# Kernel optimization log

Measured on AMD Instinct MI355X. Metric: run time of the kernel, lower is better.

Reference implementation:

```python
import jax, jax.numpy as jnp
import numpy as np

DEPTH = 4
DIM = 768
HEADS = 12
DH = 64
INNER = HEADS * DH            # 768
FF_INNER = int(4 * (2.0 / 3.0) * DIM)  # 2048 (GEGLU paper sizing)
B, N = 4, 1024                # N must be a perfect square (2D rotary)
ATTN_SCALE = 8.0              # cosine-sim attention scale from Attention(scale=8)
EPS = 1e-5


def _ln(x, gamma, beta):
    mu = jnp.mean(x, axis=-1, keepdims=True)
    var = jnp.mean((x - mu) ** 2, axis=-1, keepdims=True)
    return (x - mu) * jax.lax.rsqrt(var + EPS) * gamma + beta


def _rope_angles(n, dh):
    # precompute_freqs_cis_2d: x/y positions on sqrt(n) grid, dh//4 freqs each, interleaved
    H = int(n ** 0.5)
    pos = jnp.arange(n)
    xp = (pos % H).astype(jnp.float32)
    yp = (pos // H).astype(jnp.float32)
    freqs = 1.0 / (10000.0 ** (jnp.arange(0, dh, 4)[: dh // 4].astype(jnp.float32) / dh))
    xa = jnp.outer(xp, freqs)  # [n, dh//4]
    ya = jnp.outer(yp, freqs)
    return jnp.stack([xa, ya], axis=-1).reshape(n, dh // 2)  # [n, dh//2]


def _apply_rope(t, cos, sin):
    # t: [B, N, H, DH]; complex-pair rotation on last dim
    tr = t.reshape(*t.shape[:-1], DH // 2, 2)
    r, im = tr[..., 0], tr[..., 1]
    c = cos[None, :, None, :]
    s = sin[None, :, None, :]
    out = jnp.stack([r * c - im * s, r * s + im * c], axis=-1)
    return out.reshape(t.shape)


def _l2norm(t):
    return t / jnp.maximum(jnp.linalg.norm(t, axis=-1, keepdims=True), 1e-12)


def setup_inputs() -> dict:
    key = jax.random.key(0)
    ks = jax.random.split(key, 10)
    w = 0.02
    return {
        "x": jax.random.normal(ks[0], (B, N, DIM), dtype=jnp.float32),
        "attn_gamma": jnp.ones((DEPTH, DIM), dtype=jnp.float32),
        "wq": w * jax.random.normal(ks[1], (DEPTH, DIM, INNER), dtype=jnp.float32),
        "wkv": w * jax.random.normal(ks[2], (DEPTH, DIM, 2 * INNER), dtype=jnp.float32),
        "q_scale": jnp.ones((DEPTH, DH), dtype=jnp.float32),
        "k_scale": jnp.ones((DEPTH, DH), dtype=jnp.float32),
        "wo": w * jax.random.normal(ks[3], (DEPTH, INNER, DIM), dtype=jnp.float32),
        "ff_gamma": jnp.ones((DEPTH, DIM), dtype=jnp.float32),
        "ff_beta": jnp.zeros((DEPTH, DIM), dtype=jnp.float32),
        "wff1": w * jax.random.normal(ks[4], (DEPTH, DIM, 2 * FF_INNER), dtype=jnp.float32),
        "wff2": w * jax.random.normal(ks[5], (DEPTH, FF_INNER, DIM), dtype=jnp.float32),
    }


def reference(x, attn_gamma, wq, wkv, q_scale, k_scale, wo, ff_gamma, ff_beta, wff1, wff2):
    b, n, _ = x.shape
    ang = _rope_angles(n, DH)
    cos, sin = jnp.cos(ang), jnp.sin(ang)
    for i in range(DEPTH):
        # ---- Attention (qk-l2norm cosine attention, 2D rotary, scale=8) ----
        h = _ln(x, attn_gamma[i], 0.0)          # Attention.norm (beta is a zero buffer)
        kv_in = x                                # faithful: kv_input taken BEFORE norm
        q = (h @ wq[i]).reshape(b, n, HEADS, DH)
        kv = kv_in @ wkv[i]
        k, v = jnp.split(kv, 2, axis=-1)
        k = k.reshape(b, n, HEADS, DH)
        v = v.reshape(b, n, HEADS, DH)
        q = _apply_rope(q, cos, sin)
        k = _apply_rope(k, cos, sin)
        q = jnp.transpose(q, (0, 2, 1, 3))       # b h n d
        k = jnp.transpose(k, (0, 2, 1, 3))
        v = jnp.transpose(v, (0, 2, 1, 3))
        q = _l2norm(q) * q_scale[i]
        k = _l2norm(k) * k_scale[i]
        sim = jnp.einsum('bhid,bhjd->bhij', q, k) * ATTN_SCALE
        attn = jax.nn.softmax(sim, axis=-1)
        o = jnp.einsum('bhij,bhjd->bhid', attn, v)
        o = jnp.transpose(o, (0, 2, 1, 3)).reshape(b, n, INNER)
        x = x + o @ wo[i]
        # ---- GEGLU FeedForward ----
        hf = _ln(x, ff_gamma[i], ff_beta[i])
        u = hf @ wff1[i]
        a, g = jnp.split(u, 2, axis=-1)
        x = x + (a * jax.nn.gelu(g, approximate=False)) @ wff2[i]
    return x
```

## Files before the change

kernel.cpp:

```cpp
#include <hip/hip_runtime.h>
#include <hip/hip_bf16.h>
#include <math.h>

typedef __hip_bfloat16 bf16;
typedef __bf16 bf16x8 __attribute__((ext_vector_type(8)));
typedef float f32x4 __attribute__((ext_vector_type(4)));

#define NDEPTH 4
#define DIM 768
#define HEADS 12
#define DH 64
#define INNER 768
#define FFI 2048
#define BB 4
#define NN 1024
#define ROWS (BB*NN)

__device__ __forceinline__ void async_cp16(const bf16* g, bf16* l) {
  __builtin_amdgcn_global_load_lds(
      (const __attribute__((address_space(1))) unsigned int*)g,
      (__attribute__((address_space(3))) unsigned int*)l, 16, 0, 0);
}

template<int BN, bool GELU, bool VOUT, int K, int LD>
__device__ __forceinline__ void gemm_body(
    const bf16* __restrict__ A, const bf16* __restrict__ Bt,
    bf16* __restrict__ Cb, float* __restrict__ Cf, const float* __restrict__ Rf,
    bf16* __restrict__ Vt, int M, int N, int bx, int by, bf16* As, bf16* Bs)
{
  constexpr int WN = BN / 2;
  constexpr int NT = WN / 16;
  const int tid  = threadIdx.x;
  const int lane = tid & 63, w = tid >> 6;
  const int quad = lane >> 4, l16 = lane & 15;
  const int wr = w >> 1, wc = w & 1;
  const int m0 = by * 128, n0 = bx * BN;

  f32x4 acc[4][NT] = {};

  constexpr int CHA = 128 * 8;
  constexpr int CH  = CHA + BN * 8;
  constexpr int NCH = CH / 256;
  constexpr int NTK = K / 64;

  auto stage = [&](int kk, int buf) {
    bf16* Asb = As + buf * (128*64);
    bf16* Bsb = Bs + buf * (BN*64);
    #pragma unroll
    for (int t = 0; t < NCH; ++t) {
      int c0 = w*64 + t*256;
      int ch = c0 + lane;
      if (c0 < CHA) {
        int r = ch >> 3, j = (ch & 7) ^ (r & 7);
        async_cp16(&A[(size_t)(m0 + r)*LD + kk + j*8], &Asb[(size_t)c0*8]);
      } else {
        int ch2 = ch - CHA, r = ch2 >> 3, j = (ch2 & 7) ^ (r & 7);
        async_cp16(&Bt[(size_t)(n0 + r)*LD + kk + j*8], &Bsb[(size_t)(c0 - CHA)*8]);
      }
    }
  };

  stage(0, 0);
  __syncthreads();

  #pragma unroll
  for (int t = 0; t < NTK; ++t) {
    const int buf = t & 1;
    if (t + 1 < NTK) stage((t + 1) * 64, buf ^ 1);

    const bf16* Asb = As + buf * (128*64);
    const bf16* Bsb = Bs + buf * (BN*64);

    #pragma unroll
    for (int kc = 0; kc < 2; ++kc) {
      bf16x8 bfr[NT];
      #pragma unroll
      for (int nt = 0; nt < NT; ++nt) {
        int rb = wc*WN + nt*16 + l16;
        int c  = (kc*4 + quad) ^ (rb & 7);
        bfr[nt] = *(const bf16x8*)&Bsb[rb*64 + c*8];
      }
      #pragma unroll
      for (int mt = 0; mt < 4; ++mt) {
        int ra = wr*64 + mt*16 + l16;
        int ca = (kc*4 + quad) ^ (ra & 7);
        bf16x8 af = *(const bf16x8*)&Asb[ra*64 + ca*8];
        #pragma unroll
        for (int nt = 0; nt < NT; ++nt)
          acc[mt][nt] = __builtin_amdgcn_mfma_f32_16x16x32_bf16(af, bfr[nt], acc[mt][nt], 0, 0, 0);
      }
    }
    if (t + 1 < NTK) __syncthreads();
  }

  #pragma unroll
  for (int mt = 0; mt < 4; ++mt) {
    #pragma unroll
    for (int nt = 0; nt < NT; ++nt) {
      int row = m0 + wr*64 + mt*16 + quad*4;
      int col = n0 + wc*WN + nt*16 + l16;
      if (GELU) {
        #pragma unroll
        for (int r = 0; r < 4; ++r) {
          float v = acc[mt][nt][r];
          float g = __shfl_xor(v, 1);
          if (!(lane & 1)) {
            float ge = 0.5f * g * (1.f + erff(g * 0.70710678118654752f));
            Cb[(size_t)(row + r)*(N >> 1) + (col >> 1)] = __float2bfloat16(v * ge);
          }
        }
      } else if (VOUT) {
        if (col < INNER) {
          #pragma unroll
          for (int r = 0; r < 4; ++r)
            Cb[(size_t)(row + r)*INNER + col] = __float2bfloat16(acc[mt][nt][r]);
        } else {
          int c2 = col - INNER, hh = c2 >> 6, d = c2 & 63;
          int b = row >> 10, nn = row & 1023;
          union { ushort4 u4; bf16 h4[4]; } p;
          #pragma unroll
          for (int r = 0; r < 4; ++r) p.h4[r] = __float2bfloat16(acc[mt][nt][r]);
          *(ushort4*)&Vt[(((size_t)b*HEADS + hh)*DH + d)*NN + nn] = p.u4;
        }
      } else {
        #pragma unroll
        for (int r = 0; r < 4; ++r) {
          float v = acc[mt][nt][r];
          size_t idx = (size_t)(row + r) * N + col;
          if (Rf) v += Rf[idx];
          if (Cf) Cf[idx] = v;
          if (Cb) Cb[idx] = __float2bfloat16(v);
        }
      }
    }
  }
}

template<int BN, bool GELU, int K, int LD>
__global__ __launch_bounds__(256) void gemm_kernel(
    const bf16* __restrict__ A, const bf16* __restrict__ Bt,
    bf16* __restrict__ Cb, float* __restrict__ Cf, const float* __restrict__ Rf,
    int M, int N)
{
  __shared__ __align__(16) bf16 As[2*128*64];
  __shared__ __align__(16) bf16 Bs[2*BN*64];
  gemm_body<BN,GELU,false,K,LD>(A, Bt, Cb, Cf, Rf, nullptr, M, N,
                                blockIdx.x, blockIdx.y, As, Bs);
}

template<int BN, int KH, int LD>
__global__ __launch_bounds__(256) void gemm_splitk_kernel(
    const bf16* __restrict__ A, const bf16* __restrict__ Bt,
    float* __restrict__ P, int M, int N)
{
  __shared__ __align__(16) bf16 As[2*128*64];
  __shared__ __align__(16) bf16 Bs[2*BN*64];
  const int z = blockIdx.z;
  gemm_body<BN,false,false,KH,LD>(A + (size_t)z*KH, Bt + (size_t)z*KH, nullptr,
                                  P + (size_t)z*M*N, nullptr, nullptr,
                                  M, N, blockIdx.x, blockIdx.y, As, Bs);
}

__global__ __launch_bounds__(256) void qkv_kernel(
    const bf16* __restrict__ h, const bf16* __restrict__ x16,
    const bf16* __restrict__ wqT, const bf16* __restrict__ wkvT,
    bf16* __restrict__ qb, bf16* __restrict__ kb, bf16* __restrict__ vt)
{
  __shared__ __align__(16) bf16 As[2*128*64];
  __shared__ __align__(16) bf16 Bs[2*128*64];
  if (blockIdx.z == 0)
    gemm_body<64,false,false,768,768>(h, wqT, qb, nullptr, nullptr, nullptr,
                                      ROWS, INNER, blockIdx.x, blockIdx.y, As, Bs);
  else
    gemm_body<128,false,true,768,768>(x16, wkvT, kb, nullptr, nullptr, vt,
                                      ROWS, 2*INNER, blockIdx.x, blockIdx.y, As, Bs);
}

__global__ __launch_bounds__(256) void ln_kernel(
    const float* __restrict__ x, const float* __restrict__ g,
    const float* __restrict__ bta, bf16* __restrict__ out)
{
  const int row = blockIdx.x, tid = threadIdx.x;
  const size_t base = (size_t)row * DIM;
  float v[3];
  #pragma unroll
  for (int j = 0; j < 3; ++j) v[j] = x[base + tid + j*256];
  float s  = v[0] + v[1] + v[2];
  float ss = v[0]*v[0] + v[1]*v[1] + v[2]*v[2];
  #pragma unroll
  for (int off = 32; off; off >>= 1) { s += __shfl_xor(s, off); ss += __shfl_xor(ss, off); }
  __shared__ float red[8];
  int w = tid >> 6;
  if ((tid & 63) == 0) { red[w] = s; red[w + 4] = ss; }
  __syncthreads();
  s  = red[0] + red[1] + red[2] + red[3];
  ss = red[4] + red[5] + red[6] + red[7];
  float mean = s * (1.f/768.f);
  float var  = ss * (1.f/768.f) - mean*mean;
  float rstd = rsqrtf(fmaxf(var, 0.f) + 1e-5f);
  #pragma unroll
  for (int j = 0; j < 3; ++j) {
    int c = tid + j*256;
    float bv = bta ? bta[c] : 0.f;
    out[base + c] = __float2bfloat16((v[j] - mean) * rstd * g[c] + bv);
  }
}

__global__ __launch_bounds__(256) void redln_kernel(
    const float* __restrict__ P0, const float* __restrict__ P1,
    const float* __restrict__ res,
    float* __restrict__ xo32, bf16* __restrict__ xo16, float* __restrict__ outf,
    const float* __restrict__ g, const float* __restrict__ bta,
    bf16* __restrict__ lnout)
{
  const int row = blockIdx.x, tid = threadIdx.x;
  const size_t base = (size_t)row * DIM;
  float v[3];
  #pragma unroll
  for (int j = 0; j < 3; ++j) {
    size_t idx = base + tid + j*256;
    v[j] = res[idx] + P0[idx] + P1[idx];
    if (xo32) xo32[idx] = v[j];
    if (xo16) xo16[idx] = __float2bfloat16(v[j]);
    if (outf) outf[idx] = v[j];
  }
  if (!g) return;
  float s  = v[0] + v[1] + v[2];
  float ss = v[0]*v[0] + v[1]*v[1] + v[2]*v[2];
  #pragma unroll
  for (int off = 32; off; off >>= 1) { s += __shfl_xor(s, off); ss += __shfl_xor(ss, off); }
  __shared__ float red[8];
  int w = tid >> 6;
  if ((tid & 63) == 0) { red[w] = s; red[w + 4] = ss; }
  __syncthreads();
  s  = red[0] + red[1] + red[2] + red[3];
  ss = red[4] + red[5] + red[6] + red[7];
  float mean = s * (1.f/768.f);
  float var  = ss * (1.f/768.f) - mean*mean;
  float rstd = rsqrtf(fmaxf(var, 0.f) + 1e-5f);
  #pragma unroll
  for (int j = 0; j < 3; ++j) {
    int c = tid + j*256;
    float bv = bta ? bta[c] : 0.f;
    lnout[base + c] = __float2bfloat16((v[j] - mean) * rstd * g[c] + bv);
  }
}

__global__ __launch_bounds__(384) void rope_kernel(
    const bf16* __restrict__ q, const bf16* __restrict__ kb,
    const float* __restrict__ qsc, const float* __restrict__ ksc,
    bf16* __restrict__ qh, bf16* __restrict__ kh)
{
  const int bn = blockIdx.x;
  const int b = bn >> 10, n = bn & 1023;
  const int tid = threadIdx.x;
  const int h = tid >> 5, pr = tid & 31, d0 = pr*2;
  const float xp = (float)(n & 31), yp = (float)(n >> 5);
  const int t = pr >> 1;
  const float freq = powf(10000.f, -(float)t / 16.f);
  const float ang = (pr & 1) ? yp * freq : xp * freq;
  float sn, cs;
  sincosf(ang, &sn, &cs);
  const float2 qs2 = *(const float2*)&qsc[d0];
  const float2 ks2 = *(const float2*)&ksc[d0];

  union { unsigned int u; bf16 h2[2]; } qa, ka, qo, ko;
  qa.u = *(const unsigned int*)&q [(size_t)bn*INNER + h*64 + d0];
  ka.u = *(const unsigned int*)&kb[(size_t)bn*INNER + h*64 + d0];
  float qre = __bfloat162float(qa.h2[0]), qim = __bfloat162float(qa.h2[1]);
  float kre = __bfloat162float(ka.h2[0]), kim = __bfloat162float(ka.h2[1]);
  float qr = qre*cs - qim*sn, qi = qre*sn + qim*cs;
  float kr = kre*cs - kim*sn, ki = kre*sn + kim*cs;
  float q2 = qr*qr + qi*qi, k2 = kr*kr + ki*ki;
  #pragma unroll
  for (int off = 1; off < 32; off <<= 1) { q2 += __shfl_xor(q2, off); k2 += __shfl_xor(k2, off); }
  float qinv = 8.f / fmaxf(sqrtf(q2), 1e-12f);
  float kinv = 1.f / fmaxf(sqrtf(k2), 1e-12f);
  qo.h2[0] = __float2bfloat16(qr * qinv * qs2.x);
  qo.h2[1] = __float2bfloat16(qi * qinv * qs2.y);
  ko.h2[0] = __float2bfloat16(kr * kinv * ks2.x);
  ko.h2[1] = __float2bfloat16(ki * kinv * ks2.y);
  size_t oi = (((size_t)b*HEADS + h)*NN + n)*DH + d0;
  *(unsigned int*)&qh[oi] = qo.u;
  *(unsigned int*)&kh[oi] = ko.u;
}

__global__ __launch_bounds__(256) void attn_kernel(
    const bf16* __restrict__ qh, const bf16* __restrict__ kh,
    const bf16* __restrict__ vt, const float* __restrict__ qsc,
    const float* __restrict__ ksc, bf16* __restrict__ ob)
{
  __shared__ __align__(16) bf16 Qs[64*72];
  __shared__ __align__(16) bf16 Ks[64*72];
  __shared__ __align__(16) bf16 Vt[64*72];
  __shared__ __align__(16) bf16 Ps[4][16*72];

  const int tid = threadIdx.x;
  const int lane = tid & 63, w = tid >> 6;
  const int quad = lane >> 4, l16 = lane & 15;
  const int qt = blockIdx.x, bh = blockIdx.y;
  const int b = bh / HEADS, h = bh % HEADS;
  const size_t base = (size_t)bh * NN * DH;

  float mq = fabsf(qsc[lane]), mk = fabsf(ksc[lane]);
  #pragma unroll
  for (int off = 1; off < 64; off <<= 1) {
    mq = fmaxf(mq, __shfl_xor(mq, off));
    mk = fmaxf(mk, __shfl_xor(mk, off));
  }
  const float Mb = 8.f * mq * mk;

  for (int c = tid; c < 512; c += 256) {
    int r = c >> 3, j = c & 7;
    *(uint4*)&Qs[r*72 + j*8] = *(const uint4*)&qh[base + (size_t)(qt*64 + r)*64 + j*8];
  }

  f32x4 o[4] = {};
  float pl[4] = {0.f, 0.f, 0.f, 0.f};

  for (int kt0 = 0; kt0 < NN/64; ++kt0) {
    __syncthreads();
    for (int c = tid; c < 512; c += 256) {
      int r = c >> 3, j = c & 7;
      *(uint4*)&Ks[r*72 + j*8] = *(const uint4*)&kh[base + (size_t)(kt0*64 + r)*64 + j*8];
      *(uint4*)&Vt[r*72 + j*8] = *(const uint4*)&vt[base + (size_t)r*NN + kt0*64 + j*8];
    }
    __syncthreads();

    f32x4 s[4] = {};
    bf16x8 aq[2];
    #pragma unroll
    for (int kc = 0; kc < 2; ++kc)
      aq[kc] = *(const bf16x8*)&Qs[(w*16 + l16)*72 + kc*32 + quad*8];
    #pragma unroll
    for (int kt = 0; kt < 4; ++kt)
      #pragma unroll
      for (int kc = 0; kc < 2; ++kc) {
        bf16x8 bk = *(const bf16x8*)&Ks[(kt*16 + l16)*72 + kc*32 + quad*8];
        s[kt] = __builtin_amdgcn_mfma_f32_16x16x32_bf16(aq[kc], bk, s[kt], 0, 0, 0);
      }

    #pragma unroll
    for (int r = 0; r < 4; ++r) {
      #pragma unroll
      for (int kt = 0; kt < 4; ++kt) {
        float pv = __expf(s[kt][r] - Mb);
        pl[r] += pv;
        Ps[w][(quad*4 + r)*72 + kt*16 + l16] = __float2bfloat16(pv);
      }
    }
    __syncthreads();

    #pragma unroll
    for (int kc = 0; kc < 2; ++kc) {
      bf16x8 ap = *(const bf16x8*)&Ps[w][l16*72 + kc*32 + quad*8];
      #pragma unroll
      for (int nt = 0; nt < 4; ++nt) {
        bf16x8 bv = *(const bf16x8*)&Vt[(nt*16 + l16)*72 + kc*32 + quad*8];
        o[nt] = __builtin_amdgcn_mfma_f32_16x16x32_bf16(ap, bv, o[nt], 0, 0, 0);
      }
    }
  }

  float l[4];
  #pragma unroll
  for (int r = 0; r < 4; ++r) {
    float rs = pl[r];
    #pragma unroll
    for (int off = 1; off < 16; off <<= 1) rs += __shfl_xor(rs, off);
    l[r] = rs;
  }

  #pragma unroll
  for (int nt = 0; nt < 4; ++nt)
    #pragma unroll
    for (int r = 0; r < 4; ++r) {
      int n = qt*64 + w*16 + quad*4 + r;
      int dcol = nt*16 + l16;
      ob[((size_t)(b*NN + n)*HEADS + h)*DH + dcol] = __float2bfloat16(o[nt][r] / l[r]);
    }
}

__global__ __launch_bounds__(256) void cast_kernel(
    const float* __restrict__ x, bf16* __restrict__ o)
{
  size_t i = ((size_t)blockIdx.x*256 + threadIdx.x) * 8;
  float4 f0 = *(const float4*)(x + i);
  float4 f1 = *(const float4*)(x + i + 4);
  union { uint4 u; bf16 h[8]; } p;
  p.h[0] = __float2bfloat16(f0.x); p.h[1] = __float2bfloat16(f0.y);
  p.h[2] = __float2bfloat16(f0.z); p.h[3] = __float2bfloat16(f0.w);
  p.h[4] = __float2bfloat16(f1.x); p.h[5] = __float2bfloat16(f1.y);
  p.h[6] = __float2bfloat16(f1.z); p.h[7] = __float2bfloat16(f1.w);
  *(uint4*)(o + i) = p.u;
}

struct TD { const float* src; bf16* dst; int R, C, base, perm; };
struct TDs5 { TD d[5]; };

__global__ __launch_bounds__(256) void wtrans_kernel(TDs5 a)
{
  const int blk = blockIdx.x;
  int di = 0;
  #pragma unroll
  for (int k = 1; k < 5; ++k) if (blk >= a.d[k].base) di = k;
  const TD d = a.d[di];
  const int local = blk - d.base;
  const int tilesX = d.C >> 5;
  const int by = local / tilesX, bx = local - by*tilesX;
  __shared__ float t[32][33];
  const int tx = threadIdx.x & 31, ty = threadIdx.x >> 5;
  const int c0 = bx*32, r0 = by*32;
  #pragma unroll
  for (int i = 0; i < 4; ++i)
    t[ty + i*8][tx] = d.src[(size_t)(r0 + ty + i*8)*d.C + c0 + tx];
  __syncthreads();
  const int half = d.C >> 1;
  #pragma unroll
  for (int i = 0; i < 4; ++i) {
    int c = c0 + ty + i*8;
    int rout = d.perm ? ((c < half) ? 2*c : 2*(c - half) + 1) : c;
    d.dst[(size_t)rout*d.R + r0 + tx] = __float2bfloat16(t[tx][ty + i*8]);
  }
}

extern "C" void kernel_launch(void* const* d_in, const int* in_sizes, int n_in,
                              void* d_out, int out_size, void* d_ws, size_t ws_size,
                              hipStream_t stream)
{
  const float* x_in       = (const float*)d_in[0];
  const float* attn_gamma = (const float*)d_in[1];
  const float* wq         = (const float*)d_in[2];
  const float* wkv        = (const float*)d_in[3];
  const float* q_scale    = (const float*)d_in[4];
  const float* k_scale    = (const float*)d_in[5];
  const float* wo         = (const float*)d_in[6];
  const float* ff_gamma   = (const float*)d_in[7];
  const float* ff_beta    = (const float*)d_in[8];
  const float* wff1       = (const float*)d_in[9];
  const float* wff2       = (const float*)d_in[10];
  float* outp = (float*)d_out;
  char* ws = (char*)d_ws;

  const size_t E = (size_t)ROWS * DIM;
  float* xw32 = (float*)ws;
  bf16*  xw16 = (bf16*)(ws + 12582912);
  bf16*  S_h  = (bf16*)(ws + 18874368);
  char*  BIGb = ws + 25165824;
  bf16*  WT   = (bf16*)(ws + 62914560);
  bf16*  qbuf  = (bf16*)BIGb;
  bf16*  kbuf  = qbuf + E;
  bf16*  qhb   = qbuf + 2*E;
  bf16*  khb   = qbuf + 3*E;
  bf16*  vtb   = qbuf + 4*E;
  bf16*  glbuf = (bf16*)BIGb;
  float* wP    = (float*)BIGb;
  float* fP    = (float*)(BIGb + 16777216);
  bf16*  wqT   = WT;
  bf16*  wkvT  = WT + 589824;
  bf16*  woT   = WT + 1769472;
  bf16*  wff1T = WT + 2359296;
  bf16*  wff2T = WT + 5505024;

  cast_kernel<<<1536, 256, 0, stream>>>(x_in, xw16);
  ln_kernel<<<ROWS, 256, 0, stream>>>(x_in, attn_gamma, nullptr, S_h);

  for (int i = 0; i < NDEPTH; ++i) {
    const float* xsrc = (i == 0) ? x_in : xw32;

    TDs5 td;
    td.d[0] = { wq   + (size_t)i*589824,  wqT,   768,  768,    0, 0 };
    td.d[1] = { wkv  + (size_t)i*1179648, wkvT,  768, 1536,  576, 0 };
    td.d[2] = { wo   + (size_t)i*589824,  woT,   768,  768, 1728, 0 };
    td.d[3] = { wff1 + (size_t)i*3145728, wff1T, 768, 4096, 2304, 1 };
    td.d[4] = { wff2 + (size_t)i*1572864, wff2T, 2048, 768, 5376, 0 };
    wtrans_kernel<<<6912, 256, 0, stream>>>(td);

    qkv_kernel<<<dim3(12,32,2), 256, 0, stream>>>(S_h, xw16, wqT, wkvT, qbuf, kbuf, vtb);
    rope_kernel<<<ROWS, 384, 0, stream>>>(qbuf, kbuf, q_scale + i*DH, k_scale + i*DH, qhb, khb);
    attn_kernel<<<dim3(16,48), 256, 0, stream>>>(qhb, khb, vtb,
                                                 q_scale + i*DH, k_scale + i*DH, S_h);
    gemm_splitk_kernel<64,384,768><<<dim3(12,32,2), 256, 0, stream>>>(S_h, woT, wP, ROWS, DIM);
    redln_kernel<<<ROWS, 256, 0, stream>>>(wP, wP + E, xsrc, xw32, nullptr, nullptr,
                                           ff_gamma + i*DIM, ff_beta + i*DIM, S_h);
    gemm_kernel<128,true,768,768><<<dim3(32,32), 256, 0, stream>>>(S_h, wff1T, glbuf, nullptr, nullptr, ROWS, 2*FFI);
    gemm_splitk_kernel<64,1024,2048><<<dim3(12,32,2), 256, 0, stream>>>(glbuf, wff2T, fP, ROWS, DIM);
    if (i < NDEPTH-1)
      redln_kernel<<<ROWS, 256, 0, stream>>>(fP, fP + E, xw32, xw32, xw16, nullptr,
                                             attn_gamma + (i+1)*DIM, nullptr, S_h);
    else
      redln_kernel<<<ROWS, 256, 0, stream>>>(fP, fP + E, xw32, nullptr, nullptr, outp,
                                             nullptr, nullptr, nullptr);
  }
}
```

Measured before the change: 936.6 us.

## Triple-buffer GEMM K-loop and register-prefetch K/V tiles in attention

```diff
diff --git a/kernel.cpp b/kernel.cpp
--- a/kernel.cpp
+++ b/kernel.cpp
@@ -42,6 +42,7 @@
   constexpr int CH  = CHA + BN * 8;
   constexpr int NCH = CH / 256;
   constexpr int NTK = K / 64;
+  static_assert(NTK >= 3, "pipeline needs >=3 K-steps");
 
   auto stage = [&](int kk, int buf) {
     bf16* Asb = As + buf * (128*64);
@@ -61,12 +62,14 @@
   };
 
   stage(0, 0);
-  __syncthreads();
+  stage(64, 1);
+  asm volatile("s_waitcnt vmcnt(%0)" :: "n"(NCH) : "memory");
+  __builtin_amdgcn_s_barrier();
 
   #pragma unroll
   for (int t = 0; t < NTK; ++t) {
-    const int buf = t & 1;
-    if (t + 1 < NTK) stage((t + 1) * 64, buf ^ 1);
+    const int buf = t % 3;
+    if (t + 2 < NTK) stage((t + 2) * 64, (t + 2) % 3);
 
     const bf16* Asb = As + buf * (128*64);
     const bf16* Bsb = Bs + buf * (BN*64);
@@ -90,7 +93,14 @@
           acc[mt][nt] = __builtin_amdgcn_mfma_f32_16x16x32_bf16(af, bfr[nt], acc[mt][nt], 0, 0, 0);
       }
     }
-    if (t + 1 < NTK) __syncthreads();
+
+    if (t + 2 < NTK) {
+      asm volatile("s_waitcnt vmcnt(%0)" :: "n"(NCH) : "memory");
+      __builtin_amdgcn_s_barrier();
+    } else if (t + 1 < NTK) {
+      asm volatile("s_waitcnt vmcnt(0)" ::: "memory");
+      __builtin_amdgcn_s_barrier();
+    }
   }
 
   #pragma unroll
@@ -142,8 +152,8 @@
     bf16* __restrict__ Cb, float* __restrict__ Cf, const float* __restrict__ Rf,
     int M, int N)
 {
-  __shared__ __align__(16) bf16 As[2*128*64];
-  __shared__ __align__(16) bf16 Bs[2*BN*64];
+  __shared__ __align__(16) bf16 As[3*128*64];
+  __shared__ __align__(16) bf16 Bs[3*BN*64];
   gemm_body<BN,GELU,false,K,LD>(A, Bt, Cb, Cf, Rf, nullptr, M, N,
                                 blockIdx.x, blockIdx.y, As, Bs);
 }
@@ -153,8 +163,8 @@
     const bf16* __restrict__ A, const bf16* __restrict__ Bt,
     float* __restrict__ P, int M, int N)
 {
-  __shared__ __align__(16) bf16 As[2*128*64];
-  __shared__ __align__(16) bf16 Bs[2*BN*64];
+  __shared__ __align__(16) bf16 As[3*128*64];
+  __shared__ __align__(16) bf16 Bs[3*BN*64];
   const int z = blockIdx.z;
   gemm_body<BN,false,false,KH,LD>(A + (size_t)z*KH, Bt + (size_t)z*KH, nullptr,
                                   P + (size_t)z*M*N, nullptr, nullptr,
@@ -166,8 +176,8 @@
     const bf16* __restrict__ wqT, const bf16* __restrict__ wkvT,
     bf16* __restrict__ qb, bf16* __restrict__ kb, bf16* __restrict__ vt)
 {
-  __shared__ __align__(16) bf16 As[2*128*64];
-  __shared__ __align__(16) bf16 Bs[2*128*64];
+  __shared__ __align__(16) bf16 As[3*128*64];
+  __shared__ __align__(16) bf16 Bs[3*128*64];
   if (blockIdx.z == 0)
     gemm_body<64,false,false,768,768>(h, wqT, qb, nullptr, nullptr, nullptr,
                                       ROWS, INNER, blockIdx.x, blockIdx.y, As, Bs);
@@ -315,17 +325,33 @@
     *(uint4*)&Qs[r*72 + j*8] = *(const uint4*)&qh[base + (size_t)(qt*64 + r)*64 + j*8];
   }
 
+  uint4 krg[2], vrg[2];
+  auto ldkv = [&](int kt0) {
+    #pragma unroll
+    for (int c2 = 0; c2 < 2; ++c2) {
+      int cc = tid + c2*256, r = cc >> 3, j = cc & 7;
+      krg[c2] = *(const uint4*)&kh[base + (size_t)(kt0*64 + r)*64 + j*8];
+      vrg[c2] = *(const uint4*)&vt[base + (size_t)r*NN + kt0*64 + j*8];
+    }
+  };
+  auto stkv = [&]() {
+    #pragma unroll
+    for (int c2 = 0; c2 < 2; ++c2) {
+      int cc = tid + c2*256, r = cc >> 3, j = cc & 7;
+      *(uint4*)&Ks[r*72 + j*8] = krg[c2];
+      *(uint4*)&Vt[r*72 + j*8] = vrg[c2];
+    }
+  };
+
   f32x4 o[4] = {};
   float pl[4] = {0.f, 0.f, 0.f, 0.f};
 
+  ldkv(0);
+  stkv();
+
   for (int kt0 = 0; kt0 < NN/64; ++kt0) {
     __syncthreads();
-    for (int c = tid; c < 512; c += 256) {
-      int r = c >> 3, j = c & 7;
-      *(uint4*)&Ks[r*72 + j*8] = *(const uint4*)&kh[base + (size_t)(kt0*64 + r)*64 + j*8];
-      *(uint4*)&Vt[r*72 + j*8] = *(const uint4*)&vt[base + (size_t)r*NN + kt0*64 + j*8];
-    }
-    __syncthreads();
+    if (kt0 + 1 < NN/64) ldkv(kt0 + 1);
 
     f32x4 s[4] = {};
     bf16x8 aq[2];
@@ -349,7 +375,6 @@
         Ps[w][(quad*4 + r)*72 + kt*16 + l16] = __float2bfloat16(pv);
       }
     }
-    __syncthreads();
 
     #pragma unroll
     for (int kc = 0; kc < 2; ++kc) {
@@ -360,6 +385,9 @@
         o[nt] = __builtin_amdgcn_mfma_f32_16x16x32_bf16(ap, bv, o[nt], 0, 0, 0);
       }
     }
+
+    __syncthreads();
+    if (kt0 + 1 < NN/64) stkv();
   }
 
   float l[4];
```

Result: slower. 1.467 ms (+56.6%).

## Use 256x256-tile 512-thread GEMM for GEGLU up-projection; drop attention barrier

Applied to the files above, without the earlier changes.

```diff
diff --git a/kernel.cpp b/kernel.cpp
--- a/kernel.cpp
+++ b/kernel.cpp
@@ -136,18 +136,6 @@
   }
 }
 
-template<int BN, bool GELU, int K, int LD>
-__global__ __launch_bounds__(256) void gemm_kernel(
-    const bf16* __restrict__ A, const bf16* __restrict__ Bt,
-    bf16* __restrict__ Cb, float* __restrict__ Cf, const float* __restrict__ Rf,
-    int M, int N)
-{
-  __shared__ __align__(16) bf16 As[2*128*64];
-  __shared__ __align__(16) bf16 Bs[2*BN*64];
-  gemm_body<BN,GELU,false,K,LD>(A, Bt, Cb, Cf, Rf, nullptr, M, N,
-                                blockIdx.x, blockIdx.y, As, Bs);
-}
-
 template<int BN, int KH, int LD>
 __global__ __launch_bounds__(256) void gemm_splitk_kernel(
     const bf16* __restrict__ A, const bf16* __restrict__ Bt,
@@ -174,6 +162,88 @@
   else
     gemm_body<128,false,true,768,768>(x16, wkvT, kb, nullptr, nullptr, vt,
                                       ROWS, 2*INNER, blockIdx.x, blockIdx.y, As, Bs);
+}
+
+__global__ __launch_bounds__(512) void gemm256_kernel(
+    const bf16* __restrict__ A, const bf16* __restrict__ Bt,
+    bf16* __restrict__ Cb, int M, int N)
+{
+  __shared__ __align__(16) bf16 As[2][256*64];
+  __shared__ __align__(16) bf16 Bs[2][256*64];
+
+  const int tid  = threadIdx.x;
+  const int lane = tid & 63, wv = tid >> 6;
+  const int quad = lane >> 4, l16 = lane & 15;
+  const int wr = wv >> 2, wc = wv & 3;
+  const int m0 = blockIdx.y * 256, n0 = blockIdx.x * 256;
+
+  f32x4 acc[8][4] = {};
+
+  auto stage = [&](int kk, int buf) {
+    #pragma unroll
+    for (int t = 0; t < 8; ++t) {
+      int c0 = wv*64 + t*512;
+      int ch = c0 + lane;
+      if (c0 < 2048) {
+        int r = ch >> 3, j = (ch & 7) ^ (r & 7);
+        async_cp16(&A[(size_t)(m0 + r)*768 + kk + j*8], &As[buf][(size_t)c0*8]);
+      } else {
+        int ch2 = ch - 2048, r = ch2 >> 3, j = (ch2 & 7) ^ (r & 7);
+        async_cp16(&Bt[(size_t)(n0 + r)*768 + kk + j*8], &Bs[buf][(size_t)(c0 - 2048)*8]);
+      }
+    }
+  };
+
+  stage(0, 0);
+  __syncthreads();
+
+  #pragma unroll
+  for (int t = 0; t < 12; ++t) {
+    const int buf = t & 1;
+    if (t + 1 < 12) stage((t + 1) * 64, buf ^ 1);
+
+    const bf16* Asb = &As[buf][0];
+    const bf16* Bsb = &Bs[buf][0];
+
+    #pragma unroll
+    for (int kc = 0; kc < 2; ++kc) {
+      bf16x8 bfr[4];
+      #pragma unroll
+      for (int nt = 0; nt < 4; ++nt) {
+        int rb = wc*64 + nt*16 + l16;
+        int c  = (kc*4 + quad) ^ (rb & 7);
+        bfr[nt] = *(const bf16x8*)&Bsb[rb*64 + c*8];
+      }
+      #pragma unroll
+      for (int mt = 0; mt < 8; ++mt) {
+        int ra = wr*128 + mt*16 + l16;
+        int ca = (kc*4 + quad) ^ (ra & 7);
+        bf16x8 af = *(const bf16x8*)&Asb[ra*64 + ca*8];
+        #pragma unroll
+        for (int nt = 0; nt < 4; ++nt)
+          acc[mt][nt] = __builtin_amdgcn_mfma_f32_16x16x32_bf16(af, bfr[nt], acc[mt][nt], 0, 0, 0);
+      }
+    }
+    if (t + 1 < 12) __syncthreads();
+  }
+
+  #pragma unroll
+  for (int mt = 0; mt < 8; ++mt) {
+    #pragma unroll
+    for (int nt = 0; nt < 4; ++nt) {
+      int row = m0 + wr*128 + mt*16 + quad*4;
+      int col = n0 + wc*64 + nt*16 + l16;
+      #pragma unroll
+      for (int r = 0; r < 4; ++r) {
+        float v = acc[mt][nt][r];
+        float g = __shfl_xor(v, 1);
+        if (!(lane & 1)) {
+          float ge = 0.5f * g * (1.f + erff(g * 0.70710678118654752f));
+          Cb[(size_t)(row + r)*(N >> 1) + (col >> 1)] = __float2bfloat16(v * ge);
+        }
+      }
+    }
+  }
 }
 
 __global__ __launch_bounds__(256) void ln_kernel(
@@ -349,7 +419,6 @@
         Ps[w][(quad*4 + r)*72 + kt*16 + l16] = __float2bfloat16(pv);
       }
     }
-    __syncthreads();
 
     #pragma unroll
     for (int kc = 0; kc < 2; ++kc) {
@@ -483,7 +552,7 @@
     gemm_splitk_kernel<64,384,768><<<dim3(12,32,2), 256, 0, stream>>>(S_h, woT, wP, ROWS, DIM);
     redln_kernel<<<ROWS, 256, 0, stream>>>(wP, wP + E, xsrc, xw32, nullptr, nullptr,
                                            ff_gamma + i*DIM, ff_beta + i*DIM, S_h);
-    gemm_kernel<128,true,768,768><<<dim3(32,32), 256, 0, stream>>>(S_h, wff1T, glbuf, nullptr, nullptr, ROWS, 2*FFI);
+    gemm256_kernel<<<dim3(16,16), 512, 0, stream>>>(S_h, wff1T, glbuf, ROWS, 2*FFI);
     gemm_splitk_kernel<64,1024,2048><<<dim3(12,32,2), 256, 0, stream>>>(glbuf, wff2T, fP, ROWS, DIM);
     if (i < NDEPTH-1)
       redln_kernel<<<ROWS, 256, 0, stream>>>(fP, fP + E, xw32, xw32, xw16, nullptr,
```

Measured after the change: 936.8 us. Within noise of the previous version (+0.0%).
